# Kernel optimization log

Measured on AMD Instinct MI355X. Metric: run time of the kernel, lower is better.

Reference implementation:

```python
import jax, jax.numpy as jnp
import numpy as np
import math

B, C, H, W, D = 4, 128, 32, 32, 32
HEADS = 4
N = H * W * D            # input_size = 32768
NG = 64                  # global token count, fixed by EF1 shape (64, skip_proj)
SKIP_PROJ = C // HEADS   # 32, required by output reshape
PROJ = C // HEADS        # 32, required by attn @ v_proj contraction
LN_EPS = 1e-5


def setup_inputs() -> dict:
    key = jax.random.key(0)
    k0, k1, k2, k3, k4 = jax.random.split(key, 5)
    std1 = 1.0 / math.sqrt(SKIP_PROJ)
    std2 = 1.0 / math.sqrt(PROJ)
    return {
        "skip": jax.random.normal(k0, (B, C, H, W, D), jnp.float32),
        "out": jax.random.normal(k1, (B, C, H, W, D), jnp.float32),
        "global_fea": jax.random.normal(k2, (B, NG, C), jnp.float32),
        "ln_w": jnp.ones((C,), jnp.float32),
        "ln_b": jnp.zeros((C,), jnp.float32),
        "temperature3": jnp.ones((HEADS, 1, 1), jnp.float32),
        "EF1": jax.random.uniform(k3, (NG, SKIP_PROJ), jnp.float32, -std1, std1),
        "EF2": jax.random.uniform(k4, (N, PROJ), jnp.float32, -std2, std2),
    }


def _layernorm(x, w, b):
    mu = jnp.mean(x, axis=-1, keepdims=True)
    var = jnp.var(x, axis=-1, keepdims=True)
    return (x - mu) * jax.lax.rsqrt(var + LN_EPS) * w + b


def reference(skip, out, global_fea, ln_w, ln_b, temperature3, EF1, EF2):
    b, c, h_, w_, d_ = skip.shape
    n = h_ * w_ * d_
    nh = temperature3.shape[0]
    dh = c // nh
    # (B,C,H,W,D) -> (B,N,C)
    skip_t = skip.reshape(b, c, n).transpose(0, 2, 1)
    out_t = out.reshape(b, c, n).transpose(0, 2, 1)
    skip_n = _layernorm(skip_t, ln_w, ln_b)
    out_n = _layernorm(out_t, ln_w, ln_b)
    # heads: (B,N,C) -> (B,h,d,N)
    q = out_n.reshape(b, n, nh, dh).transpose(0, 2, 3, 1)
    k = skip_n.reshape(b, n, nh, dh).transpose(0, 2, 3, 1)
    v = global_fea.reshape(b, -1, nh, dh).transpose(0, 2, 3, 1)  # (B,h,d,NG)
    v_proj = jnp.einsum('bhdn,nk->bhdk', v, EF1)   # (B,h,d,SKIP_PROJ)
    k_proj = jnp.einsum('bhdn,nk->bhdk', k, EF2)   # (B,h,d,PROJ)
    # q^T k_proj: (B,h,N,PROJ), scaled by per-head temperature
    attn = jnp.einsum('bhdn,bhdp->bhnp', q, k_proj) * temperature3
    attn = jax.nn.softmax(attn, axis=-1)
    # attn @ v_proj contracts PROJ with the d axis of v_proj (PROJ == d)
    x = jnp.einsum('bhnp,bhpk->bhnk', attn, v_proj)   # (B,h,N,SKIP_PROJ)
    x = x.transpose(0, 3, 1, 2).reshape(b, n, c)       # (B,N,C)
    # (B,N,C) -> (B,C,H,W,D)
    return x.reshape(b, h_, w_, d_, c).transpose(0, 4, 1, 2, 3)
```

## Files before the change

kernel.cpp:

```cpp
#include <hip/hip_runtime.h>
#include <hip/hip_bf16.h>

#define NN 32768
#define LN_EPS 1e-5f

typedef float v4f __attribute__((ext_vector_type(4)));
typedef __attribute__((ext_vector_type(8))) short bf16x8;
typedef __attribute__((ext_vector_type(4))) float f32x4;

__device__ __forceinline__ void bsplit(float f, short &hi, short &lo) {
  unsigned u; __builtin_memcpy(&u, &f, 4);
  unsigned hb = u & 0xffff0000u;
  hi = (short)(u >> 16);
  float hf; __builtin_memcpy(&hf, &hb, 4);
  float lf = f - hf;
  unsigned ul; __builtin_memcpy(&ul, &lf, 4);
  lo = (short)(ul >> 16);
}

__device__ __forceinline__ unsigned short bf16u(float f) {
  unsigned u; __builtin_memcpy(&u, &f, 4);
  return (unsigned short)(u >> 16);
}

__global__ __launch_bounds__(256) void k1_mfma(
    const float* __restrict__ skip, const float* __restrict__ EF2,
    float* __restrict__ partials)
{
  __shared__ float cred[4752];

  int bx = blockIdx.x, t = threadIdx.x;
  int b = bx >> 7, chunk = bx & 127;
  int w = t >> 6, l = t & 63;
  int i16 = l & 15, kc = (l >> 4) << 3;

  f32x4 acc[9][2];
#pragma unroll
  for (int mt = 0; mt < 9; ++mt)
#pragma unroll
    for (int nt = 0; nt < 2; ++nt)
      acc[mt][nt] = (f32x4){0.f, 0.f, 0.f, 0.f};

#pragma unroll
  for (int it = 0; it < 2; ++it) {
    int n0 = chunk * 256 + w * 64 + it * 32;
    int kt = chunk * 8 + w * 2 + it;

    bf16x8 Bh[2], Bl[2];
    const float* eb = EF2 + (size_t)(kt * 32 + kc) * 32;
#pragma unroll
    for (int nt = 0; nt < 2; ++nt) {
#pragma unroll
      for (int j = 0; j < 8; ++j) {
        float e = eb[(size_t)j * 32 + nt * 16 + i16];
        short hh, ll; bsplit(e, hh, ll);
        Bh[nt][j] = hh; Bl[nt][j] = ll;
      }
    }

    const float* ap = skip + (size_t)(b * 128) * NN + n0 + kc;
    float af[8][8];
#pragma unroll
    for (int mt = 0; mt < 8; ++mt) {
      const float* rp = ap + (size_t)(mt * 16 + i16) * NN;
      float4 a0 = *(const float4*)(rp);
      float4 a1 = *(const float4*)(rp + 4);
      af[mt][0] = a0.x; af[mt][1] = a0.y; af[mt][2] = a0.z; af[mt][3] = a0.w;
      af[mt][4] = a1.x; af[mt][5] = a1.y; af[mt][6] = a1.z; af[mt][7] = a1.w;
    }

    float cs[8], sq[8];
#pragma unroll
    for (int j = 0; j < 8; ++j) {
      float s = 0.f, q = 0.f;
#pragma unroll
      for (int mt = 0; mt < 8; ++mt) { s += af[mt][j]; q = fmaf(af[mt][j], af[mt][j], q); }
      cs[j] = s; sq[j] = q;
    }
#pragma unroll
    for (int m = 1; m <= 8; m <<= 1) {
#pragma unroll
      for (int j = 0; j < 8; ++j) {
        cs[j] += __shfl_xor(cs[j], m);
        sq[j] += __shfl_xor(sq[j], m);
      }
    }
    float rs[8], mr[8];
#pragma unroll
    for (int j = 0; j < 8; ++j) {
      float mu = cs[j] * (1.f / 128.f);
      rs[j] = rsqrtf(sq[j] * (1.f / 128.f) - mu * mu + LN_EPS);
      mr[j] = mu * rs[j];
    }

#pragma unroll
    for (int mt = 0; mt < 8; ++mt) {
      bf16x8 Ah, Al;
#pragma unroll
      for (int j = 0; j < 8; ++j) {
        short h, lo; bsplit(af[mt][j] * rs[j], h, lo);
        Ah[j] = h; Al[j] = lo;
      }
#pragma unroll
      for (int nt = 0; nt < 2; ++nt) {
        acc[mt][nt] = __builtin_amdgcn_mfma_f32_16x16x32_bf16(Ah, Bh[nt], acc[mt][nt], 0, 0, 0);
        acc[mt][nt] = __builtin_amdgcn_mfma_f32_16x16x32_bf16(Al, Bh[nt], acc[mt][nt], 0, 0, 0);
        acc[mt][nt] = __builtin_amdgcn_mfma_f32_16x16x32_bf16(Ah, Bl[nt], acc[mt][nt], 0, 0, 0);
      }
    }
    {
      bf16x8 Ah, Al;
#pragma unroll
      for (int j = 0; j < 8; ++j) {
        float v = (i16 == 0) ? mr[j] : ((i16 == 1) ? 1.f : 0.f);
        short h, lo; bsplit(v, h, lo);
        Ah[j] = h; Al[j] = lo;
      }
#pragma unroll
      for (int nt = 0; nt < 2; ++nt) {
        acc[8][nt] = __builtin_amdgcn_mfma_f32_16x16x32_bf16(Ah, Bh[nt], acc[8][nt], 0, 0, 0);
        acc[8][nt] = __builtin_amdgcn_mfma_f32_16x16x32_bf16(Al, Bh[nt], acc[8][nt], 0, 0, 0);
        acc[8][nt] = __builtin_amdgcn_mfma_f32_16x16x32_bf16(Ah, Bl[nt], acc[8][nt], 0, 0, 0);
      }
    }
  }

  int rbase = (l >> 4) * 4;
  for (int ww = 0; ww < 4; ++ww) {
    __syncthreads();
    if (w == ww) {
#pragma unroll
      for (int mt = 0; mt < 9; ++mt)
#pragma unroll
        for (int nt = 0; nt < 2; ++nt)
#pragma unroll
          for (int r = 0; r < 4; ++r) {
            int addr = (mt * 16 + rbase + r) * 33 + nt * 16 + i16;
            if (ww == 0) cred[addr] = acc[mt][nt][r];
            else         cred[addr] += acc[mt][nt][r];
          }
    }
  }
  __syncthreads();
  float* pw = partials + (size_t)bx * 4608;
#pragma unroll
  for (int i = 0; i < 18; ++i) {
    int idx = t + i * 256;
    pw[idx] = cred[(idx >> 5) * 33 + (idx & 31)];
  }
}

__global__ __launch_bounds__(256) void k2_red(
    const float* __restrict__ partials, float* __restrict__ raw)
{
  __shared__ float red[8][32];
  int row = blockIdx.x;
  int b   = blockIdx.y;
  int t = threadIdx.x;
  int p = t & 31, grp = t >> 5;
  const float* pp = partials + ((size_t)(b * 128 + grp * 16)) * 4608 + row * 32 + p;
  float s = 0.f;
  for (int i = 0; i < 16; ++i)
    s += pp[(size_t)i * 4608];
  red[grp][p] = s;
  __syncthreads();
  if (t < 32) {
    float tot = 0.f;
#pragma unroll
    for (int g2 = 0; g2 < 8; ++g2) tot += red[g2][t];
    raw[((size_t)b * 130 + row) * 32 + t] = tot;
  }
}

__global__ __launch_bounds__(64) void k2_post(
    const float* __restrict__ raw, const float* __restrict__ gf,
    const float* __restrict__ EF1, const float* __restrict__ lnw,
    const float* __restrict__ lnb,
    float* __restrict__ W1, float* __restrict__ B1,
    short* __restrict__ kfrag, short* __restrict__ vfrag)
{
  __shared__ float kpw_s[32][33];
  __shared__ float vps_s[32][33];
  int bh = blockIdx.x, l = threadIdx.x;
  int b = bh >> 2, h = bh & 3;
  int p = l & 31, half = l >> 5;
  const float* rb = raw + (size_t)b * 130 * 32;
  float T = rb[128 * 32 + p];
  float U = rb[129 * 32 + p];
  float w1a = 0.f, b1a = 0.f;
#pragma unroll
  for (int d2 = 0; d2 < 16; ++d2) {
    int d = half * 16 + d2, c = h * 32 + d;
    float tot = rb[c * 32 + p];
    float kp = lnw[c] * (tot - T) + lnb[c] * U;
    float kw = lnw[c] * kp;
    kpw_s[d][p] = kw;
    w1a += kw;
    b1a += lnb[c] * kp;
  }
  w1a += __shfl_xor(w1a, 32);
  b1a += __shfl_xor(b1a, 32);
  if (half == 0) {
    W1[bh * 32 + p] = w1a;
    B1[bh * 32 + p] = b1a;
  }
  {
    float acc[16];
#pragma unroll
    for (int kk = 0; kk < 16; ++kk) acc[kk] = 0.f;
    for (int g = 0; g < 64; ++g) {
      float gv = gf[((size_t)(b * 64 + g)) * 128 + h * 32 + p];
      const float* e1 = EF1 + g * 32 + half * 16;
#pragma unroll
      for (int kk = 0; kk < 16; ++kk) acc[kk] += gv * e1[kk];
    }
#pragma unroll
    for (int kk = 0; kk < 16; ++kk) vps_s[p][half * 16 + kk] = acc[kk];
  }
  __syncthreads();
  int i16 = l & 15, g4 = l >> 4;
#pragma unroll
  for (int pt = 0; pt < 2; ++pt) {
    bf16x8 hi8, lo8;
#pragma unroll
    for (int j = 0; j < 8; ++j) {
      short hh, ll; bsplit(kpw_s[g4 * 8 + j][pt * 16 + i16], hh, ll);
      hi8[j] = hh; lo8[j] = ll;
    }
    *(bf16x8*)(kfrag + (size_t)bh * 2048 + pt * 1024 + l * 8) = hi8;
    *(bf16x8*)(kfrag + (size_t)bh * 2048 + pt * 1024 + 512 + l * 8) = lo8;
  }
#pragma unroll
  for (int kt = 0; kt < 2; ++kt) {
    bf16x8 hi8, lo8;
#pragma unroll
    for (int j = 0; j < 8; ++j) {
      short hh, ll; bsplit(vps_s[g4 * 8 + j][kt * 16 + i16], hh, ll);
      hi8[j] = hh; lo8[j] = ll;
    }
    *(bf16x8*)(vfrag + (size_t)bh * 2048 + kt * 1024 + l * 8) = hi8;
    *(bf16x8*)(vfrag + (size_t)bh * 2048 + kt * 1024 + 512 + l * 8) = lo8;
  }
}

__global__ __launch_bounds__(256) void k3_attn(
    const float* __restrict__ outp, const short* __restrict__ kfrag,
    const short* __restrict__ vfrag, const float* __restrict__ W1,
    const float* __restrict__ B1, const float* __restrict__ temp,
    __hip_bfloat16* __restrict__ xws)
{
  __shared__ float q_lds[4128];
  __shared__ float2 sst[32];
  __shared__ unsigned short p_lds[2304];

  int bx = blockIdx.x, t = threadIdx.x;
  int w = t >> 6, l = t & 63;
  int b = bx >> 10, chunk = bx & 1023;
  int n0 = chunk * 32;
  int i16 = l & 15, g4 = l >> 4;

  const float* qb = outp + (size_t)b * 128 * NN + n0;
  int nq = (t & 7) * 4, cb = t >> 3;
#pragma unroll
  for (int pass = 0; pass < 4; ++pass) {
    int c = pass * 32 + cb;
    float4 v = *(const float4*)(qb + (size_t)c * NN + nq);
    q_lds[(nq + 0) * 129 + c] = v.x;
    q_lds[(nq + 1) * 129 + c] = v.y;
    q_lds[(nq + 2) * 129 + c] = v.z;
    q_lds[(nq + 3) * 129 + c] = v.w;
  }
  __syncthreads();

  {
    int g8 = l >> 3, r8 = l & 7;
    int row = w * 8 + r8;
    const float* qrow = &q_lds[row * 129 + g8 * 16];
    float s = 0.f, q2s = 0.f;
#pragma unroll
    for (int st2 = 0; st2 < 16; ++st2) {
      int cc = (st2 + 4 * g8) & 15;
      float v = qrow[cc];
      s += v; q2s = fmaf(v, v, q2s);
    }
    s += __shfl_xor(s, 8);  q2s += __shfl_xor(q2s, 8);
    s += __shfl_xor(s, 16); q2s += __shfl_xor(q2s, 16);
    s += __shfl_xor(s, 32); q2s += __shfl_xor(q2s, 32);
    if (g8 == 0) {
      float mu = s * (1.f / 128.f);
      float rs = rsqrtf(q2s * (1.f / 128.f) - mu * mu + LN_EPS);
      sst[row] = make_float2(mu, rs);
    }
  }
  __syncthreads();

  int h = w;
  const short* kfb = kfrag + (size_t)((b * 4 + h) * 2048);
  const short* vfb = vfrag + (size_t)((b * 4 + h) * 2048);
  bf16x8 KAh[2], KAl[2], VAh[2], VAl[2];
#pragma unroll
  for (int pt = 0; pt < 2; ++pt) {
    KAh[pt] = *(const bf16x8*)(kfb + pt * 1024 + l * 8);
    KAl[pt] = *(const bf16x8*)(kfb + pt * 1024 + 512 + l * 8);
    VAh[pt] = *(const bf16x8*)(vfb + pt * 1024 + l * 8);
    VAl[pt] = *(const bf16x8*)(vfb + pt * 1024 + 512 + l * 8);
  }
  float w1v[8], b1v[8];
#pragma unroll
  for (int pt = 0; pt < 2; ++pt)
#pragma unroll
    for (int r = 0; r < 4; ++r) {
      int p = g4 * 4 + r + pt * 16;
      w1v[pt * 4 + r] = W1[(b * 4 + h) * 32 + p];
      b1v[pt * 4 + r] = B1[(b * 4 + h) * 32 + p];
    }
  float tm = temp[h];
  unsigned short* pwv = p_lds + w * 576;
  __hip_bfloat16* xwb = xws + ((size_t)((b * 4 + h) * 32) << 15) + n0 + i16;

#pragma unroll
  for (int nt2 = 0; nt2 < 2; ++nt2) {
    int nrow = nt2 * 16 + i16;
    float2 mr = sst[nrow];

    bf16x8 QBh, QBl;
#pragma unroll
    for (int j = 0; j < 8; ++j) {
      float v = q_lds[nrow * 129 + h * 32 + g4 * 8 + j];
      short hh, ll; bsplit(v, hh, ll);
      QBh[j] = hh; QBl[j] = ll;
    }

    f32x4 C[2];
#pragma unroll
    for (int pt = 0; pt < 2; ++pt) {
      C[pt] = (f32x4){0.f, 0.f, 0.f, 0.f};
      C[pt] = __builtin_amdgcn_mfma_f32_16x16x32_bf16(KAh[pt], QBh, C[pt], 0, 0, 0);
      C[pt] = __builtin_amdgcn_mfma_f32_16x16x32_bf16(KAl[pt], QBh, C[pt], 0, 0, 0);
      C[pt] = __builtin_amdgcn_mfma_f32_16x16x32_bf16(KAh[pt], QBl, C[pt], 0, 0, 0);
    }

    float lg[8];
#pragma unroll
    for (int pt = 0; pt < 2; ++pt)
#pragma unroll
      for (int r = 0; r < 4; ++r)
        lg[pt * 4 + r] = tm * (mr.y * C[pt][r] - mr.y * mr.x * w1v[pt * 4 + r] + b1v[pt * 4 + r]);
    float mx = lg[0];
#pragma unroll
    for (int i = 1; i < 8; ++i) mx = fmaxf(mx, lg[i]);
    mx = fmaxf(mx, __shfl_xor(mx, 16));
    mx = fmaxf(mx, __shfl_xor(mx, 32));
    float sum = 0.f;
#pragma unroll
    for (int i = 0; i < 8; ++i) { float e = __expf(lg[i] - mx); lg[i] = e; sum += e; }
    sum += __shfl_xor(sum, 16);
    sum += __shfl_xor(sum, 32);
    float inv = 1.f / sum;
#pragma unroll
    for (int i = 0; i < 8; ++i) lg[i] *= inv;

#pragma unroll
    for (int pt = 0; pt < 2; ++pt)
#pragma unroll
      for (int r = 0; r < 4; ++r)
        pwv[(pt * 16 + g4 * 4 + r) * 18 + i16] = bf16u(lg[pt * 4 + r]);
    __builtin_amdgcn_wave_barrier();
    bf16x8 PBh;
#pragma unroll
    for (int j = 0; j < 8; ++j)
      PBh[j] = (short)pwv[(g4 * 8 + j) * 18 + i16];
    __builtin_amdgcn_wave_barrier();

    f32x4 X[2];
#pragma unroll
    for (int kt = 0; kt < 2; ++kt) {
      X[kt] = (f32x4){0.f, 0.f, 0.f, 0.f};
      X[kt] = __builtin_amdgcn_mfma_f32_16x16x32_bf16(VAh[kt], PBh, X[kt], 0, 0, 0);
      X[kt] = __builtin_amdgcn_mfma_f32_16x16x32_bf16(VAl[kt], PBh, X[kt], 0, 0, 0);
    }

    __hip_bfloat16* xw = xwb + nt2 * 16;
#pragma unroll
    for (int kt = 0; kt < 2; ++kt)
#pragma unroll
      for (int r = 0; r < 4; ++r) {
        int k = kt * 16 + g4 * 4 + r;
        xw[(size_t)k << 15] = __float2bfloat16(X[kt][r]);
      }
  }
}

__global__ __launch_bounds__(256) void k4_scatter(
    const __hip_bfloat16* __restrict__ xws, float* __restrict__ outd)
{
  __shared__ float tile[64][129];
  int bx = blockIdx.x;
  int tg = bx & 3;
  int k = (bx >> 2) & 31;
  int h = (bx >> 7) & 3;
  int b = bx >> 9;
  int t = threadIdx.x;
  const __hip_bfloat16* src = xws + ((size_t)((b * 4 + h) * 32 + k) << 15) + tg * 64 * 128;
  for (int idx = t; idx < 64 * 128; idx += 256) {
    int nh = idx >> 7, c0 = idx & 127;
    tile[nh][c0] = __bfloat162float(src[idx]);
  }
  __syncthreads();
  int nh = t & 63, cq = t >> 6;
  size_t obase = (size_t)b * 128 * NN + (size_t)k * 1024 + h * 256 + tg * 64 + nh;
  for (int i = 0; i < 32; ++i) {
    int c0 = i * 4 + cq;
    outd[obase + (size_t)c0 * NN] = tile[nh][c0];
  }
}

extern "C" void kernel_launch(void* const* d_in, const int* in_sizes, int n_in,
                              void* d_out, int out_size, void* d_ws, size_t ws_size,
                              hipStream_t stream) {
  const float* skip = (const float*)d_in[0];
  const float* outp = (const float*)d_in[1];
  const float* gf   = (const float*)d_in[2];
  const float* lnw  = (const float*)d_in[3];
  const float* lnb  = (const float*)d_in[4];
  const float* temp = (const float*)d_in[5];
  const float* EF1  = (const float*)d_in[6];
  const float* EF2  = (const float*)d_in[7];
  float* outd = (float*)d_out;
  char* ws = (char*)d_ws;

  __hip_bfloat16* xws = (__hip_bfloat16*)ws;
  float* partials = (float*)ws;
  float* raw   = outd + 524288;
  float* W1    = outd + 540928;
  float* B1    = outd + 541440;
  short* kfrag = (short*)(outd + 541952);
  short* vfrag = (short*)(outd + 558336);

  k1_mfma<<<512, 256, 0, stream>>>(skip, EF2, partials);
  k2_red<<<dim3(130, 4), 256, 0, stream>>>(partials, raw);
  k2_post<<<16, 64, 0, stream>>>(raw, gf, EF1, lnw, lnb, W1, B1, kfrag, vfrag);
  k3_attn<<<4096, 256, 0, stream>>>(outp, kfrag, vfrag, W1, B1, temp, xws);
  k4_scatter<<<2048, 256, 0, stream>>>(xws, outd);
}
```

Before: 74.14 us.

## Make attention blocks persistent over four chunks with register prefetch of q

The attention kernel now has each block process four 32-token chunks instead of one, cutting the grid from 4096 to 1024 blocks. The per-head K/V fragments, W1/B1 and temperature are loaded once per block and reused across the chunks. The next chunk's q tile is prefetched into registers while the current chunk computes. LDS is double-buffered, at the cost of more shared memory, extra barriers and fewer resident blocks.

```diff
diff --git a/kernel.cpp b/kernel.cpp
--- a/kernel.cpp
+++ b/kernel.cpp
@@ -249,33 +249,60 @@
     const float* __restrict__ B1, const float* __restrict__ temp,
     __hip_bfloat16* __restrict__ xws)
 {
-  __shared__ float q_lds[4128];
-  __shared__ float2 sst[32];
+  __shared__ float q_lds[2][4128];
+  __shared__ float2 sst[2][32];
   __shared__ unsigned short p_lds[2304];
 
   int bx = blockIdx.x, t = threadIdx.x;
   int w = t >> 6, l = t & 63;
-  int b = bx >> 10, chunk = bx & 1023;
-  int n0 = chunk * 32;
+  int b = bx >> 8, sc = bx & 255;
   int i16 = l & 15, g4 = l >> 4;
-
-  const float* qb = outp + (size_t)b * 128 * NN + n0;
   int nq = (t & 7) * 4, cb = t >> 3;
+
+  const float* qbase = outp + (size_t)b * 128 * NN + sc * 128;
+
+  float4 rg[4];
+#pragma unroll
+  for (int pass = 0; pass < 4; ++pass)
+    rg[pass] = *(const float4*)(qbase + (size_t)(pass * 32 + cb) * NN + nq);
+
+  int h = w;
+  const short* kfb = kfrag + (size_t)((b * 4 + h) * 2048);
+  const short* vfb = vfrag + (size_t)((b * 4 + h) * 2048);
+  bf16x8 KAh[2], KAl[2], VAh[2], VAl[2];
+#pragma unroll
+  for (int pt = 0; pt < 2; ++pt) {
+    KAh[pt] = *(const bf16x8*)(kfb + pt * 1024 + l * 8);
+    KAl[pt] = *(const bf16x8*)(kfb + pt * 1024 + 512 + l * 8);
+    VAh[pt] = *(const bf16x8*)(vfb + pt * 1024 + l * 8);
+    VAl[pt] = *(const bf16x8*)(vfb + pt * 1024 + 512 + l * 8);
+  }
+  float w1v[8], b1v[8];
+#pragma unroll
+  for (int pt = 0; pt < 2; ++pt)
+#pragma unroll
+    for (int r = 0; r < 4; ++r) {
+      int p = g4 * 4 + r + pt * 16;
+      w1v[pt * 4 + r] = W1[(b * 4 + h) * 32 + p];
+      b1v[pt * 4 + r] = B1[(b * 4 + h) * 32 + p];
+    }
+  float tm = temp[h];
+  unsigned short* pwv = p_lds + w * 576;
+  __hip_bfloat16* xwh = xws + ((size_t)((b * 4 + h) * 32) << 15) + sc * 128 + i16;
+
 #pragma unroll
   for (int pass = 0; pass < 4; ++pass) {
     int c = pass * 32 + cb;
-    float4 v = *(const float4*)(qb + (size_t)c * NN + nq);
-    q_lds[(nq + 0) * 129 + c] = v.x;
-    q_lds[(nq + 1) * 129 + c] = v.y;
-    q_lds[(nq + 2) * 129 + c] = v.z;
-    q_lds[(nq + 3) * 129 + c] = v.w;
-  }
-  __syncthreads();
-
+    q_lds[0][(nq + 0) * 129 + c] = rg[pass].x;
+    q_lds[0][(nq + 1) * 129 + c] = rg[pass].y;
+    q_lds[0][(nq + 2) * 129 + c] = rg[pass].z;
+    q_lds[0][(nq + 3) * 129 + c] = rg[pass].w;
+  }
+  __syncthreads();
   {
     int g8 = l >> 3, r8 = l & 7;
     int row = w * 8 + r8;
-    const float* qrow = &q_lds[row * 129 + g8 * 16];
+    const float* qrow = &q_lds[0][row * 129 + g8 * 16];
     float s = 0.f, q2s = 0.f;
 #pragma unroll
     for (int st2 = 0; st2 < 16; ++st2) {
@@ -288,106 +315,128 @@
     s += __shfl_xor(s, 32); q2s += __shfl_xor(q2s, 32);
     if (g8 == 0) {
       float mu = s * (1.f / 128.f);
-      float rs = rsqrtf(q2s * (1.f / 128.f) - mu * mu + LN_EPS);
-      sst[row] = make_float2(mu, rs);
-    }
-  }
-  __syncthreads();
-
-  int h = w;
-  const short* kfb = kfrag + (size_t)((b * 4 + h) * 2048);
-  const short* vfb = vfrag + (size_t)((b * 4 + h) * 2048);
-  bf16x8 KAh[2], KAl[2], VAh[2], VAl[2];
-#pragma unroll
-  for (int pt = 0; pt < 2; ++pt) {
-    KAh[pt] = *(const bf16x8*)(kfb + pt * 1024 + l * 8);
-    KAl[pt] = *(const bf16x8*)(kfb + pt * 1024 + 512 + l * 8);
-    VAh[pt] = *(const bf16x8*)(vfb + pt * 1024 + l * 8);
-    VAl[pt] = *(const bf16x8*)(vfb + pt * 1024 + 512 + l * 8);
-  }
-  float w1v[8], b1v[8];
-#pragma unroll
-  for (int pt = 0; pt < 2; ++pt)
-#pragma unroll
-    for (int r = 0; r < 4; ++r) {
-      int p = g4 * 4 + r + pt * 16;
-      w1v[pt * 4 + r] = W1[(b * 4 + h) * 32 + p];
-      b1v[pt * 4 + r] = B1[(b * 4 + h) * 32 + p];
-    }
-  float tm = temp[h];
-  unsigned short* pwv = p_lds + w * 576;
-  __hip_bfloat16* xwb = xws + ((size_t)((b * 4 + h) * 32) << 15) + n0 + i16;
-
-#pragma unroll
-  for (int nt2 = 0; nt2 < 2; ++nt2) {
-    int nrow = nt2 * 16 + i16;
-    float2 mr = sst[nrow];
-
-    bf16x8 QBh, QBl;
-#pragma unroll
-    for (int j = 0; j < 8; ++j) {
-      float v = q_lds[nrow * 129 + h * 32 + g4 * 8 + j];
-      short hh, ll; bsplit(v, hh, ll);
-      QBh[j] = hh; QBl[j] = ll;
-    }
-
-    f32x4 C[2];
-#pragma unroll
-    for (int pt = 0; pt < 2; ++pt) {
-      C[pt] = (f32x4){0.f, 0.f, 0.f, 0.f};
-      C[pt] = __builtin_amdgcn_mfma_f32_16x16x32_bf16(KAh[pt], QBh, C[pt], 0, 0, 0);
-      C[pt] = __builtin_amdgcn_mfma_f32_16x16x32_bf16(KAl[pt], QBh, C[pt], 0, 0, 0);
-      C[pt] = __builtin_amdgcn_mfma_f32_16x16x32_bf16(KAh[pt], QBl, C[pt], 0, 0, 0);
-    }
-
-    float lg[8];
-#pragma unroll
-    for (int pt = 0; pt < 2; ++pt)
-#pragma unroll
-      for (int r = 0; r < 4; ++r)
-        lg[pt * 4 + r] = tm * (mr.y * C[pt][r] - mr.y * mr.x * w1v[pt * 4 + r] + b1v[pt * 4 + r]);
-    float mx = lg[0];
-#pragma unroll
-    for (int i = 1; i < 8; ++i) mx = fmaxf(mx, lg[i]);
-    mx = fmaxf(mx, __shfl_xor(mx, 16));
-    mx = fmaxf(mx, __shfl_xor(mx, 32));
-    float sum = 0.f;
-#pragma unroll
-    for (int i = 0; i < 8; ++i) { float e = __expf(lg[i] - mx); lg[i] = e; sum += e; }
-    sum += __shfl_xor(sum, 16);
-    sum += __shfl_xor(sum, 32);
-    float inv = 1.f / sum;
-#pragma unroll
-    for (int i = 0; i < 8; ++i) lg[i] *= inv;
-
-#pragma unroll
-    for (int pt = 0; pt < 2; ++pt)
-#pragma unroll
-      for (int r = 0; r < 4; ++r)
-        pwv[(pt * 16 + g4 * 4 + r) * 18 + i16] = bf16u(lg[pt * 4 + r]);
-    __builtin_amdgcn_wave_barrier();
-    bf16x8 PBh;
-#pragma unroll
-    for (int j = 0; j < 8; ++j)
-      PBh[j] = (short)pwv[(g4 * 8 + j) * 18 + i16];
-    __builtin_amdgcn_wave_barrier();
-
-    f32x4 X[2];
-#pragma unroll
-    for (int kt = 0; kt < 2; ++kt) {
-      X[kt] = (f32x4){0.f, 0.f, 0.f, 0.f};
-      X[kt] = __builtin_amdgcn_mfma_f32_16x16x32_bf16(VAh[kt], PBh, X[kt], 0, 0, 0);
-      X[kt] = __builtin_amdgcn_mfma_f32_16x16x32_bf16(VAl[kt], PBh, X[kt], 0, 0, 0);
-    }
-
-    __hip_bfloat16* xw = xwb + nt2 * 16;
-#pragma unroll
-    for (int kt = 0; kt < 2; ++kt)
-#pragma unroll
-      for (int r = 0; r < 4; ++r) {
-        int k = kt * 16 + g4 * 4 + r;
-        xw[(size_t)k << 15] = __float2bfloat16(X[kt][r]);
-      }
+      float rsv = rsqrtf(q2s * (1.f / 128.f) - mu * mu + LN_EPS);
+      sst[0][row] = make_float2(mu, rsv);
+    }
+  }
+  __syncthreads();
+
+#pragma unroll
+  for (int j = 0; j < 4; ++j) {
+    int buf = j & 1;
+    if (j < 3) {
+#pragma unroll
+      for (int pass = 0; pass < 4; ++pass)
+        rg[pass] = *(const float4*)(qbase + (size_t)(pass * 32 + cb) * NN + (j + 1) * 32 + nq);
+    }
+
+    const float* ql = &q_lds[buf][0];
+#pragma unroll
+    for (int nt2 = 0; nt2 < 2; ++nt2) {
+      int nrow = nt2 * 16 + i16;
+      float2 mr = sst[buf][nrow];
+
+      bf16x8 QBh, QBl;
+#pragma unroll
+      for (int jj = 0; jj < 8; ++jj) {
+        float v = ql[nrow * 129 + h * 32 + g4 * 8 + jj];
+        short hh, ll; bsplit(v, hh, ll);
+        QBh[jj] = hh; QBl[jj] = ll;
+      }
+
+      f32x4 C[2];
+#pragma unroll
+      for (int pt = 0; pt < 2; ++pt) {
+        C[pt] = (f32x4){0.f, 0.f, 0.f, 0.f};
+        C[pt] = __builtin_amdgcn_mfma_f32_16x16x32_bf16(KAh[pt], QBh, C[pt], 0, 0, 0);
+        C[pt] = __builtin_amdgcn_mfma_f32_16x16x32_bf16(KAl[pt], QBh, C[pt], 0, 0, 0);
+        C[pt] = __builtin_amdgcn_mfma_f32_16x16x32_bf16(KAh[pt], QBl, C[pt], 0, 0, 0);
+      }
+
+      float lg[8];
+#pragma unroll
+      for (int pt = 0; pt < 2; ++pt)
+#pragma unroll
+        for (int r = 0; r < 4; ++r)
+          lg[pt * 4 + r] = tm * (mr.y * C[pt][r] - mr.y * mr.x * w1v[pt * 4 + r] + b1v[pt * 4 + r]);
+      float mx = lg[0];
+#pragma unroll
+      for (int i = 1; i < 8; ++i) mx = fmaxf(mx, lg[i]);
+      mx = fmaxf(mx, __shfl_xor(mx, 16));
+      mx = fmaxf(mx, __shfl_xor(mx, 32));
+      float sum = 0.f;
+#pragma unroll
+      for (int i = 0; i < 8; ++i) { float e = __expf(lg[i] - mx); lg[i] = e; sum += e; }
+      sum += __shfl_xor(sum, 16);
+      sum += __shfl_xor(sum, 32);
+      float inv = 1.f / sum;
+#pragma unroll
+      for (int i = 0; i < 8; ++i) lg[i] *= inv;
+
+#pragma unroll
+      for (int pt = 0; pt < 2; ++pt)
+#pragma unroll
+        for (int r = 0; r < 4; ++r)
+          pwv[(pt * 16 + g4 * 4 + r) * 18 + i16] = bf16u(lg[pt * 4 + r]);
+      __builtin_amdgcn_wave_barrier();
+      bf16x8 PBh;
+#pragma unroll
+      for (int jj = 0; jj < 8; ++jj)
+        PBh[jj] = (short)pwv[(g4 * 8 + jj) * 18 + i16];
+      __builtin_amdgcn_wave_barrier();
+
+      f32x4 X[2];
+#pragma unroll
+      for (int kt = 0; kt < 2; ++kt) {
+        X[kt] = (f32x4){0.f, 0.f, 0.f, 0.f};
+        X[kt] = __builtin_amdgcn_mfma_f32_16x16x32_bf16(VAh[kt], PBh, X[kt], 0, 0, 0);
+        X[kt] = __builtin_amdgcn_mfma_f32_16x16x32_bf16(VAl[kt], PBh, X[kt], 0, 0, 0);
+      }
+
+      __hip_bfloat16* xw = xwh + j * 32 + nt2 * 16;
+#pragma unroll
+      for (int kt = 0; kt < 2; ++kt)
+#pragma unroll
+        for (int r = 0; r < 4; ++r) {
+          int k = kt * 16 + g4 * 4 + r;
+          xw[(size_t)k << 15] = __float2bfloat16(X[kt][r]);
+        }
+    }
+
+    if (j < 3) {
+      int nb = (j + 1) & 1;
+      __syncthreads();
+#pragma unroll
+      for (int pass = 0; pass < 4; ++pass) {
+        int c = pass * 32 + cb;
+        q_lds[nb][(nq + 0) * 129 + c] = rg[pass].x;
+        q_lds[nb][(nq + 1) * 129 + c] = rg[pass].y;
+        q_lds[nb][(nq + 2) * 129 + c] = rg[pass].z;
+        q_lds[nb][(nq + 3) * 129 + c] = rg[pass].w;
+      }
+      __syncthreads();
+      {
+        int g8 = l >> 3, r8 = l & 7;
+        int row = w * 8 + r8;
+        const float* qrow = &q_lds[nb][row * 129 + g8 * 16];
+        float s = 0.f, q2s = 0.f;
+#pragma unroll
+        for (int st2 = 0; st2 < 16; ++st2) {
+          int cc = (st2 + 4 * g8) & 15;
+          float v = qrow[cc];
+          s += v; q2s = fmaf(v, v, q2s);
+        }
+        s += __shfl_xor(s, 8);  q2s += __shfl_xor(q2s, 8);
+        s += __shfl_xor(s, 16); q2s += __shfl_xor(q2s, 16);
+        s += __shfl_xor(s, 32); q2s += __shfl_xor(q2s, 32);
+        if (g8 == 0) {
+          float mu = s * (1.f / 128.f);
+          float rsv = rsqrtf(q2s * (1.f / 128.f) - mu * mu + LN_EPS);
+          sst[nb][row] = make_float2(mu, rsv);
+        }
+      }
+      __syncthreads();
+    }
   }
 }
 
@@ -440,6 +489,6 @@
   k1_mfma<<<512, 256, 0, stream>>>(skip, EF2, partials);
   k2_red<<<dim3(130, 4), 256, 0, stream>>>(partials, raw);
   k2_post<<<16, 64, 0, stream>>>(raw, gf, EF1, lnw, lnb, W1, B1, kfrag, vfrag);
-  k3_attn<<<4096, 256, 0, stream>>>(outp, kfrag, vfrag, W1, B1, temp, xws);
+  k3_attn<<<1024, 256, 0, stream>>>(outp, kfrag, vfrag, W1, B1, temp, xws);
   k4_scatter<<<2048, 256, 0, stream>>>(xws, outd);
 }
```

Measured after the change: 75.21 us. About the same (+1.4%).

## Fuse layernorm stats into Q load, pack bf16 stores and LDS traffic

Applied to the files above, without the earlier changes.

Computes the per-token layernorm sum and sum-of-squares while loading Q from global memory, using shuffles and a small cross-wave LDS reduction, instead of re-reading the transposed tile. It pads the Q tile to a 132-float stride so each lane can read its Q row with float4 loads. The P matrix goes through LDS as packed pairs of bf16 in 32-bit words, and the two 16-row output halves are kept in registers and written together as packed 32-bit stores. The scatter kernel reads 32-bit words and unpacks them to match the new interleaved intermediate layout. This adds register pressure from holding both output tiles and couples the two kernels to a permuted workspace layout.

```diff
diff --git a/kernel.cpp b/kernel.cpp
--- a/kernel.cpp
+++ b/kernel.cpp
@@ -249,48 +249,52 @@
     const float* __restrict__ B1, const float* __restrict__ temp,
     __hip_bfloat16* __restrict__ xws)
 {
-  __shared__ float q_lds[4128];
+  __shared__ float q_lds[32 * 132];
   __shared__ float2 sst[32];
-  __shared__ unsigned short p_lds[2304];
+  __shared__ float sstp[4][2][32];
+  __shared__ unsigned p32[4][272];
 
   int bx = blockIdx.x, t = threadIdx.x;
   int w = t >> 6, l = t & 63;
   int b = bx >> 10, chunk = bx & 1023;
   int n0 = chunk * 32;
   int i16 = l & 15, g4 = l >> 4;
+  int nq = (t & 7) * 4, cb = t >> 3;
 
   const float* qb = outp + (size_t)b * 128 * NN + n0;
-  int nq = (t & 7) * 4, cb = t >> 3;
+  float s4[4] = {0.f, 0.f, 0.f, 0.f}, q24[4] = {0.f, 0.f, 0.f, 0.f};
 #pragma unroll
   for (int pass = 0; pass < 4; ++pass) {
     int c = pass * 32 + cb;
     float4 v = *(const float4*)(qb + (size_t)c * NN + nq);
-    q_lds[(nq + 0) * 129 + c] = v.x;
-    q_lds[(nq + 1) * 129 + c] = v.y;
-    q_lds[(nq + 2) * 129 + c] = v.z;
-    q_lds[(nq + 3) * 129 + c] = v.w;
-  }
-  __syncthreads();
-
-  {
-    int g8 = l >> 3, r8 = l & 7;
-    int row = w * 8 + r8;
-    const float* qrow = &q_lds[row * 129 + g8 * 16];
-    float s = 0.f, q2s = 0.f;
-#pragma unroll
-    for (int st2 = 0; st2 < 16; ++st2) {
-      int cc = (st2 + 4 * g8) & 15;
-      float v = qrow[cc];
-      s += v; q2s = fmaf(v, v, q2s);
-    }
-    s += __shfl_xor(s, 8);  q2s += __shfl_xor(q2s, 8);
-    s += __shfl_xor(s, 16); q2s += __shfl_xor(q2s, 16);
-    s += __shfl_xor(s, 32); q2s += __shfl_xor(q2s, 32);
-    if (g8 == 0) {
-      float mu = s * (1.f / 128.f);
-      float rs = rsqrtf(q2s * (1.f / 128.f) - mu * mu + LN_EPS);
-      sst[row] = make_float2(mu, rs);
-    }
+    q_lds[(nq + 0) * 132 + c] = v.x;
+    q_lds[(nq + 1) * 132 + c] = v.y;
+    q_lds[(nq + 2) * 132 + c] = v.z;
+    q_lds[(nq + 3) * 132 + c] = v.w;
+    s4[0] += v.x; q24[0] = fmaf(v.x, v.x, q24[0]);
+    s4[1] += v.y; q24[1] = fmaf(v.y, v.y, q24[1]);
+    s4[2] += v.z; q24[2] = fmaf(v.z, v.z, q24[2]);
+    s4[3] += v.w; q24[3] = fmaf(v.w, v.w, q24[3]);
+  }
+#pragma unroll
+  for (int m = 8; m <= 32; m <<= 1) {
+#pragma unroll
+    for (int k = 0; k < 4; ++k) {
+      s4[k] += __shfl_xor(s4[k], m);
+      q24[k] += __shfl_xor(q24[k], m);
+    }
+  }
+  if ((l & 56) == 0) {
+    *(float4*)&sstp[w][0][nq] = (float4){s4[0], s4[1], s4[2], s4[3]};
+    *(float4*)&sstp[w][1][nq] = (float4){q24[0], q24[1], q24[2], q24[3]};
+  }
+  __syncthreads();
+  if (t < 32) {
+    float s  = sstp[0][0][t] + sstp[1][0][t] + sstp[2][0][t] + sstp[3][0][t];
+    float q2 = sstp[0][1][t] + sstp[1][1][t] + sstp[2][1][t] + sstp[3][1][t];
+    float mu = s * (1.f / 128.f);
+    float rsv = rsqrtf(q2 * (1.f / 128.f) - mu * mu + LN_EPS);
+    sst[t] = make_float2(mu, rsv);
   }
   __syncthreads();
 
@@ -315,20 +319,23 @@
       b1v[pt * 4 + r] = B1[(b * 4 + h) * 32 + p];
     }
   float tm = temp[h];
-  unsigned short* pwv = p_lds + w * 576;
-  __hip_bfloat16* xwb = xws + ((size_t)((b * 4 + h) * 32) << 15) + n0 + i16;
+  unsigned* pwv = &p32[w][0];
+  f32x4 Xs[2][2];
 
 #pragma unroll
   for (int nt2 = 0; nt2 < 2; ++nt2) {
     int nrow = nt2 * 16 + i16;
     float2 mr = sst[nrow];
 
+    const float* qrow = &q_lds[nrow * 132 + h * 32 + g4 * 8];
+    float4 qa = *(const float4*)(qrow);
+    float4 qb4 = *(const float4*)(qrow + 4);
+    float qf[8] = {qa.x, qa.y, qa.z, qa.w, qb4.x, qb4.y, qb4.z, qb4.w};
     bf16x8 QBh, QBl;
 #pragma unroll
-    for (int j = 0; j < 8; ++j) {
-      float v = q_lds[nrow * 129 + h * 32 + g4 * 8 + j];
-      short hh, ll; bsplit(v, hh, ll);
-      QBh[j] = hh; QBl[j] = ll;
+    for (int jj = 0; jj < 8; ++jj) {
+      short hh, ll; bsplit(qf[jj], hh, ll);
+      QBh[jj] = hh; QBl[jj] = ll;
     }
 
     f32x4 C[2];
@@ -363,32 +370,39 @@
 #pragma unroll
     for (int pt = 0; pt < 2; ++pt)
 #pragma unroll
-      for (int r = 0; r < 4; ++r)
-        pwv[(pt * 16 + g4 * 4 + r) * 18 + i16] = bf16u(lg[pt * 4 + r]);
+      for (int pr = 0; pr < 2; ++pr) {
+        unsigned wlo = bf16u(lg[pt * 4 + pr * 2]);
+        unsigned whi = bf16u(lg[pt * 4 + pr * 2 + 1]);
+        pwv[(pt * 8 + g4 * 2 + pr) * 17 + i16] = (whi << 16) | wlo;
+      }
     __builtin_amdgcn_wave_barrier();
     bf16x8 PBh;
 #pragma unroll
-    for (int j = 0; j < 8; ++j)
-      PBh[j] = (short)pwv[(g4 * 8 + j) * 18 + i16];
+    for (int jw = 0; jw < 4; ++jw) {
+      unsigned wv = pwv[(g4 * 4 + jw) * 17 + i16];
+      PBh[2 * jw]     = (short)(wv & 0xffffu);
+      PBh[2 * jw + 1] = (short)(wv >> 16);
+    }
     __builtin_amdgcn_wave_barrier();
 
-    f32x4 X[2];
 #pragma unroll
     for (int kt = 0; kt < 2; ++kt) {
-      X[kt] = (f32x4){0.f, 0.f, 0.f, 0.f};
-      X[kt] = __builtin_amdgcn_mfma_f32_16x16x32_bf16(VAh[kt], PBh, X[kt], 0, 0, 0);
-      X[kt] = __builtin_amdgcn_mfma_f32_16x16x32_bf16(VAl[kt], PBh, X[kt], 0, 0, 0);
-    }
-
-    __hip_bfloat16* xw = xwb + nt2 * 16;
-#pragma unroll
-    for (int kt = 0; kt < 2; ++kt)
-#pragma unroll
-      for (int r = 0; r < 4; ++r) {
-        int k = kt * 16 + g4 * 4 + r;
-        xw[(size_t)k << 15] = __float2bfloat16(X[kt][r]);
-      }
-  }
+      f32x4 X = (f32x4){0.f, 0.f, 0.f, 0.f};
+      X = __builtin_amdgcn_mfma_f32_16x16x32_bf16(VAh[kt], PBh, X, 0, 0, 0);
+      X = __builtin_amdgcn_mfma_f32_16x16x32_bf16(VAl[kt], PBh, X, 0, 0, 0);
+      Xs[nt2][kt] = X;
+    }
+  }
+
+  short* xwb = (short*)xws + (((size_t)((b * 4 + h) * 32)) << 15) + n0 + i16 * 2;
+#pragma unroll
+  for (int kt = 0; kt < 2; ++kt)
+#pragma unroll
+    for (int r = 0; r < 4; ++r) {
+      int k = kt * 16 + g4 * 4 + r;
+      unsigned pkd = ((unsigned)bf16u(Xs[1][kt][r]) << 16) | (unsigned)bf16u(Xs[0][kt][r]);
+      *(unsigned*)(xwb + ((size_t)k << 15)) = pkd;
+    }
 }
 
 __global__ __launch_bounds__(256) void k4_scatter(
@@ -401,10 +415,18 @@
   int h = (bx >> 7) & 3;
   int b = bx >> 9;
   int t = threadIdx.x;
-  const __hip_bfloat16* src = xws + ((size_t)((b * 4 + h) * 32 + k) << 15) + tg * 64 * 128;
-  for (int idx = t; idx < 64 * 128; idx += 256) {
-    int nh = idx >> 7, c0 = idx & 127;
-    tile[nh][c0] = __bfloat162float(src[idx]);
+  const unsigned* src32 = (const unsigned*)((const short*)xws +
+      (((size_t)((b * 4 + h) * 32 + k)) << 15) + tg * 8192);
+  for (int i2 = t; i2 < 4096; i2 += 256) {
+    unsigned v = src32[i2];
+    int loc = ((i2 >> 4) << 5) | (i2 & 15);
+    unsigned lo = v & 0xffffu, hi = v >> 16;
+    __hip_bfloat16 blo, bhi;
+    __builtin_memcpy(&blo, &lo, 2);
+    __builtin_memcpy(&bhi, &hi, 2);
+    tile[loc >> 7][loc & 127] = __bfloat162float(blo);
+    int loc2 = loc + 16;
+    tile[loc2 >> 7][loc2 & 127] = __bfloat162float(bhi);
   }
   __syncthreads();
   int nh = t & 63, cq = t >> 6;
```

New measurement: 73.43 us. Within noise of the previous version (-1.0%).
